# Kernel tuning notes

Measured on AMD Instinct MI355X. Metric: run time of the kernel, lower is better.

Reference implementation:

```python
import jax, jax.numpy as jnp
import numpy as np
from jax import lax

E4M3 = jnp.float8_e4m3fn
DIM_NUMS = (((1,), (0,)), ((), ()))  # contract inputs last dim with kernel first dim


def quantize_dequantize(x, q_dtype, scale, compute_dtype):
    dtype_max = jnp.finfo(q_dtype).max.astype(compute_dtype)
    s = scale.astype(compute_dtype)
    scaled = x.astype(compute_dtype) / s
    clipped = jnp.clip(scaled, -dtype_max, dtype_max)
    qx = clipped.astype(q_dtype)
    # dequantize back to x.dtype
    return qx.astype(x.dtype) * scale.astype(x.dtype)


def setup_inputs() -> dict:
    key = jax.random.key(0)
    k1, k2 = jax.random.split(key)
    H = 1024  # amax_history_length
    return {
        "inputs": jax.random.normal(k1, (8192, 4096), dtype=jnp.float32),
        "kernel": jax.random.normal(k2, (4096, 4096), dtype=jnp.float32),
        "input_scale": jnp.ones((1,), jnp.float32),
        "input_amax_history": jnp.zeros((H,), jnp.float32),
        "kernel_scale": jnp.ones((1,), jnp.float32),
        "kernel_amax_history": jnp.zeros((H,), jnp.float32),
        "output_grad_scale": jnp.ones((1,), jnp.float32),
        "output_grad_amax_history": jnp.zeros((H,), jnp.float32),
    }


def reference(inputs, kernel, input_scale, input_amax_history, kernel_scale,
              kernel_amax_history, output_grad_scale, output_grad_amax_history):
    comp_dtype = kernel.dtype
    inputs = jnp.asarray(inputs, comp_dtype)
    # in_qdq on both operands (e4m3); out_qdq is identity in the forward pass.
    lhs_qdq = quantize_dequantize(inputs, E4M3, input_scale, comp_dtype)
    rhs_qdq = quantize_dequantize(kernel, E4M3, kernel_scale, comp_dtype)
    out = lax.dot_general(lhs_qdq, rhs_qdq, DIM_NUMS, precision=None)
    return out
```

## Files before the change

kernel.cpp:

```cpp
#include <hip/hip_runtime.h>
#include <stdint.h>

#define M_DIM 8192
#define N_DIM 4096
#define K_DIM 4096
#define NT (K_DIM / 128)

typedef float f32x4 __attribute__((ext_vector_type(4)));
typedef float f32x16 __attribute__((ext_vector_type(16)));
typedef int v4i __attribute__((ext_vector_type(4)));
typedef int v8i __attribute__((ext_vector_type(8)));
typedef uint32_t u32;


__device__ __forceinline__ void gload_lds16(const void* g, void* l) {
  __builtin_amdgcn_global_load_lds(
      (__attribute__((address_space(1))) void*)(g),
      (__attribute__((address_space(3))) void*)(l), 16, 0, 0);
}

__device__ __forceinline__ float clipdiv(float v, float s) {
  v = v / s;
  return fminf(fmaxf(v, -448.f), 448.f);
}

__device__ __forceinline__ u32 pack4_fp8(float a, float b, float c, float d) {
  int w = __builtin_amdgcn_cvt_pk_fp8_f32(a, b, 0, false);
  w = __builtin_amdgcn_cvt_pk_fp8_f32(c, d, w, true);
  return (u32)w;
}

__device__ __forceinline__ v8i rd8(const void* lo, const void* hi) {
  v4i l = *(const v4i*)lo;
  v4i h = *(const v4i*)hi;
  return __builtin_shufflevector(l, h, 0, 1, 2, 3, 4, 5, 6, 7);
}

__device__ __forceinline__ f32x16 mfma32(v8i a, v8i b, f32x16 c) {
  return __builtin_amdgcn_mfma_scale_f32_32x32x64_f8f6f4(
      a, b, c, 0, 0, 0, 0x7f7f7f7f, 0, 0x7f7f7f7f);
}


__global__ __launch_bounds__(256) void quant_a(const float* __restrict__ x,
                                               u32* __restrict__ q,
                                               const float* __restrict__ scale,
                                               int nv4) {
  int base = blockIdx.x * 1024 + threadIdx.x;
  float s = scale[0];
#pragma unroll
  for (int r = 0; r < 4; ++r) {
    int idx = base + r * 256;
    if (idx < nv4) {
      float4 v = ((const float4*)x)[idx];
      q[idx] = pack4_fp8(clipdiv(v.x, s), clipdiv(v.y, s),
                         clipdiv(v.z, s), clipdiv(v.w, s));
    }
  }
}


__global__ __launch_bounds__(256) void quant_b_t(const float* __restrict__ B,
                                                 uint8_t* __restrict__ qT,
                                                 const float* __restrict__ scale) {
  __shared__ u32 lt[64 * 17];
  int tid = threadIdx.x;
  int kt = blockIdx.x * 64;
  int nt = blockIdx.y * 64;
  float s = scale[0];

  int kq = tid >> 4;
  int nq = tid & 15;
  int k0 = kq * 4, n0 = nq * 4;
  const float* src = B + (long)(kt + k0) * N_DIM + nt + n0;
  float4 v0 = *(const float4*)(src);
  float4 v1 = *(const float4*)(src + N_DIM);
  float4 v2 = *(const float4*)(src + 2 * N_DIM);
  float4 v3 = *(const float4*)(src + 3 * N_DIM);

  lt[(n0 + 0) * 17 + kq] = pack4_fp8(clipdiv(v0.x, s), clipdiv(v1.x, s),
                                     clipdiv(v2.x, s), clipdiv(v3.x, s));
  lt[(n0 + 1) * 17 + kq] = pack4_fp8(clipdiv(v0.y, s), clipdiv(v1.y, s),
                                     clipdiv(v2.y, s), clipdiv(v3.y, s));
  lt[(n0 + 2) * 17 + kq] = pack4_fp8(clipdiv(v0.z, s), clipdiv(v1.z, s),
                                     clipdiv(v2.z, s), clipdiv(v3.z, s));
  lt[(n0 + 3) * 17 + kq] = pack4_fp8(clipdiv(v0.w, s), clipdiv(v1.w, s),
                                     clipdiv(v2.w, s), clipdiv(v3.w, s));
  __syncthreads();

  int n = tid >> 2, ch = tid & 3;
  uint4 o;
  o.x = lt[n * 17 + ch * 4 + 0];
  o.y = lt[n * 17 + ch * 4 + 1];
  o.z = lt[n * 17 + ch * 4 + 2];
  o.w = lt[n * 17 + ch * 4 + 3];
  *(uint4*)&qT[(long)(nt + n) * K_DIM + kt + ch * 16] = o;
}


template <int BUF>
__device__ __forceinline__ void stage_tile(const uint8_t* const (&gA)[4],
                                           const uint8_t* const (&gB)[4],
                                           uint8_t* lds, const int (&ldo)[4],
                                           long ko) {
#pragma unroll
  for (int r = 0; r < 4; ++r)
    gload_lds16(gA[r] + ko, lds + BUF * 32768 + ldo[r]);
#pragma unroll
  for (int r = 0; r < 4; ++r)
    gload_lds16(gB[r] + ko, lds + 65536 + BUF * 32768 + ldo[r]);
}

template <int BUF>
__device__ __forceinline__ void compute_tile(const uint8_t* lds,
                                             const int (&offA)[4][4],
                                             const int (&offB)[2][4],
                                             f32x16 (&acc)[4][2]) {
  const uint8_t* Ab = lds + BUF * 32768;
  const uint8_t* Bb = lds + 65536 + BUF * 32768;
#pragma unroll
  for (int ks = 0; ks < 2; ++ks) {
    v8i b[2], a[4];
#pragma unroll
    for (int nj = 0; nj < 2; ++nj)
      b[nj] = rd8(Bb + offB[nj][ks * 2], Bb + offB[nj][ks * 2 + 1]);
#pragma unroll
    for (int mi = 0; mi < 4; ++mi)
      a[mi] = rd8(Ab + offA[mi][ks * 2], Ab + offA[mi][ks * 2 + 1]);
#pragma unroll
    for (int mi = 0; mi < 4; ++mi)
#pragma unroll
      for (int nj = 0; nj < 2; ++nj)
        acc[mi][nj] = mfma32(a[mi], b[nj], acc[mi][nj]);
  }
}

__global__ __launch_bounds__(512, 2) void gemm_mx(const uint8_t* __restrict__ Aq,
                                                  const uint8_t* __restrict__ BqT,
                                                  float* __restrict__ C,
                                                  const float* __restrict__ sA,
                                                  const float* __restrict__ sB) {
  __shared__ __align__(16) uint8_t lds[131072];

  const int tid = threadIdx.x;
  const int lane = tid & 63;
  const int wid = tid >> 6;
  const int wr = wid >> 2;
  const int wc = wid & 3;
  const int l31 = lane & 31;
  const int hi2 = lane >> 5;

  int bid = blockIdx.x;
  int wg = (bid & 7) * 64 + (bid >> 3);
  const long bm = (long)(wg >> 4) * 256;
  const long bn = (long)(wg & 15) * 256;

  float s = sA[0] * sB[0];
  asm volatile("" ::"v"(s));

  const uint8_t* gA[4];
  const uint8_t* gB[4];
  int ldo[4];
#pragma unroll
  for (int r = 0; r < 4; ++r) {
    int gid = tid + 512 * r;
    int row = gid >> 3, gc = gid & 7;
    int sc = (gc ^ (row & 7)) << 4;
    gA[r] = Aq + (bm + row) * (long)K_DIM + sc;
    gB[r] = BqT + (bn + row) * (long)K_DIM + sc;
    ldo[r] = gid * 16;
  }

  int offA[4][4], offB[2][4];
#pragma unroll
  for (int mi = 0; mi < 4; ++mi) {
    int ra = wr * 128 + mi * 32 + l31;
#pragma unroll
    for (int ks = 0; ks < 2; ++ks)
#pragma unroll
      for (int j = 0; j < 2; ++j) {
        int g = ks * 4 + hi2 * 2 + j;
        offA[mi][ks * 2 + j] = ra * 128 + ((g ^ (ra & 7)) << 4);
      }
  }
#pragma unroll
  for (int nj = 0; nj < 2; ++nj) {
    int rb = wc * 64 + nj * 32 + l31;
#pragma unroll
    for (int ks = 0; ks < 2; ++ks)
#pragma unroll
      for (int j = 0; j < 2; ++j) {
        int g = ks * 4 + hi2 * 2 + j;
        offB[nj][ks * 2 + j] = rb * 128 + ((g ^ (rb & 7)) << 4);
      }
  }

  f32x16 acc[4][2] = {};

  stage_tile<0>(gA, gB, lds, ldo, 0);
  asm volatile("s_waitcnt vmcnt(0)" ::: "memory");
  __builtin_amdgcn_s_barrier();

  for (int i = 0; i < NT / 2; ++i) {
    long ko1 = (long)((2 * i + 1) & (NT - 1)) * 128;
    stage_tile<1>(gA, gB, lds, ldo, ko1);
    compute_tile<0>(lds, offA, offB, acc);
    asm volatile("s_waitcnt vmcnt(0)" ::: "memory");
    __builtin_amdgcn_s_barrier();

    long ko2 = (long)((2 * i + 2) & (NT - 1)) * 128;
    stage_tile<0>(gA, gB, lds, ldo, ko2);
    compute_tile<1>(lds, offA, offB, acc);
    asm volatile("s_waitcnt vmcnt(0)" ::: "memory");
    __builtin_amdgcn_s_barrier();
  }

#pragma unroll
  for (int mi = 0; mi < 4; ++mi)
#pragma unroll
    for (int nj = 0; nj < 2; ++nj) {
      f32x16 v = acc[mi][nj];
      long col = bn + wc * 64 + nj * 32 + l31;
#pragma unroll
      for (int q = 0; q < 16; ++q) {
        long row = bm + wr * 128 + mi * 32 + (q & 3) + 8 * (q >> 2) + 4 * hi2;
        C[row * N_DIM + col] = v[q] * s;
      }
    }
}


extern "C" void kernel_launch(void* const* d_in, const int* in_sizes, int n_in,
                              void* d_out, int out_size, void* d_ws, size_t ws_size,
                              hipStream_t stream) {
  const float* A = (const float*)d_in[0];
  const float* B = (const float*)d_in[1];
  const float* sA = (const float*)d_in[2];
  const float* sB = (const float*)d_in[4];
  float* out = (float*)d_out;

  uint8_t* Aq = (uint8_t*)d_ws;
  uint8_t* BqT = Aq + (size_t)M_DIM * K_DIM;

  int nv4_a = M_DIM * K_DIM / 4;
  quant_a<<<nv4_a / 1024, 256, 0, stream>>>(A, (u32*)Aq, sA, nv4_a);
  quant_b_t<<<dim3(K_DIM / 64, N_DIM / 64), 256, 0, stream>>>(B, BqT, sB);
  gemm_mx<<<dim3((M_DIM / 256) * (N_DIM / 256)), 512, 0, stream>>>(Aq, BqT, out, sA, sB);
}
```

Baseline: 189.1 us.

## Interleave split global-to-LDS loads with MFMA phases using barriers and setprio

Splits each K-tile into two half-phases. Each phase issues half of the next tile's global-to-LDS loads (A first, then B), reads LDS fragments, meets at a workgroup barrier, then runs the MFMAs at raised wave priority. The aim is to spread memory traffic across the tile and keep waves in lockstep so MFMA bursts and loads from co-resident waves overlap better. The cost is extra barriers per tile and stricter scheduling constraints from sched_barrier.

```diff
diff --git a/kernel.cpp b/kernel.cpp
--- a/kernel.cpp
+++ b/kernel.cpp
@@ -99,39 +99,62 @@
 
 
 template <int BUF>
-__device__ __forceinline__ void stage_tile(const uint8_t* const (&gA)[4],
-                                           const uint8_t* const (&gB)[4],
-                                           uint8_t* lds, const int (&ldo)[4],
-                                           long ko) {
-#pragma unroll
-  for (int r = 0; r < 4; ++r)
-    gload_lds16(gA[r] + ko, lds + BUF * 32768 + ldo[r]);
-#pragma unroll
-  for (int r = 0; r < 4; ++r)
-    gload_lds16(gB[r] + ko, lds + 65536 + BUF * 32768 + ldo[r]);
-}
-
-template <int BUF>
-__device__ __forceinline__ void compute_tile(const uint8_t* lds,
-                                             const int (&offA)[4][4],
-                                             const int (&offB)[2][4],
-                                             f32x16 (&acc)[4][2]) {
+__device__ __forceinline__ void ktile(uint8_t* lds, const uint8_t* const (&gA)[4],
+                                      const uint8_t* const (&gB)[4],
+                                      const int (&ldo)[4], long ko_next,
+                                      const int (&offA)[4][4],
+                                      const int (&offB)[2][4],
+                                      f32x16 (&acc)[4][2]) {
   const uint8_t* Ab = lds + BUF * 32768;
   const uint8_t* Bb = lds + 65536 + BUF * 32768;
-#pragma unroll
-  for (int ks = 0; ks < 2; ++ks) {
-    v8i b[2], a[4];
+
+  {
+#pragma unroll
+    for (int r = 0; r < 4; ++r)
+      gload_lds16(gA[r] + ko_next, lds + (BUF ^ 1) * 32768 + ldo[r]);
+    v8i a[4], b[2];
 #pragma unroll
     for (int nj = 0; nj < 2; ++nj)
-      b[nj] = rd8(Bb + offB[nj][ks * 2], Bb + offB[nj][ks * 2 + 1]);
-#pragma unroll
-    for (int mi = 0; mi < 4; ++mi)
-      a[mi] = rd8(Ab + offA[mi][ks * 2], Ab + offA[mi][ks * 2 + 1]);
+      b[nj] = rd8(Bb + offB[nj][0], Bb + offB[nj][1]);
+#pragma unroll
+    for (int mi = 0; mi < 4; ++mi)
+      a[mi] = rd8(Ab + offA[mi][0], Ab + offA[mi][1]);
+    __builtin_amdgcn_s_barrier();
+    asm volatile("s_waitcnt lgkmcnt(0)" ::: "memory");
+    __builtin_amdgcn_sched_barrier(0);
+    __builtin_amdgcn_s_setprio(1);
 #pragma unroll
     for (int mi = 0; mi < 4; ++mi)
 #pragma unroll
       for (int nj = 0; nj < 2; ++nj)
         acc[mi][nj] = mfma32(a[mi], b[nj], acc[mi][nj]);
+    __builtin_amdgcn_s_setprio(0);
+    __builtin_amdgcn_s_barrier();
+  }
+
+  {
+#pragma unroll
+    for (int r = 0; r < 4; ++r)
+      gload_lds16(gB[r] + ko_next, lds + 65536 + (BUF ^ 1) * 32768 + ldo[r]);
+    v8i a[4], b[2];
+#pragma unroll
+    for (int nj = 0; nj < 2; ++nj)
+      b[nj] = rd8(Bb + offB[nj][2], Bb + offB[nj][3]);
+#pragma unroll
+    for (int mi = 0; mi < 4; ++mi)
+      a[mi] = rd8(Ab + offA[mi][2], Ab + offA[mi][3]);
+    __builtin_amdgcn_s_barrier();
+    asm volatile("s_waitcnt lgkmcnt(0)" ::: "memory");
+    __builtin_amdgcn_sched_barrier(0);
+    __builtin_amdgcn_s_setprio(1);
+#pragma unroll
+    for (int mi = 0; mi < 4; ++mi)
+#pragma unroll
+      for (int nj = 0; nj < 2; ++nj)
+        acc[mi][nj] = mfma32(a[mi], b[nj], acc[mi][nj]);
+    __builtin_amdgcn_s_setprio(0);
+    asm volatile("s_waitcnt vmcnt(0)" ::: "memory");
+    __builtin_amdgcn_s_barrier();
   }
 }
 
@@ -197,22 +220,18 @@
 
   f32x16 acc[4][2] = {};
 
-  stage_tile<0>(gA, gB, lds, ldo, 0);
+#pragma unroll
+  for (int r = 0; r < 4; ++r) gload_lds16(gA[r], lds + ldo[r]);
+#pragma unroll
+  for (int r = 0; r < 4; ++r) gload_lds16(gB[r], lds + 65536 + ldo[r]);
   asm volatile("s_waitcnt vmcnt(0)" ::: "memory");
   __builtin_amdgcn_s_barrier();
 
   for (int i = 0; i < NT / 2; ++i) {
     long ko1 = (long)((2 * i + 1) & (NT - 1)) * 128;
-    stage_tile<1>(gA, gB, lds, ldo, ko1);
-    compute_tile<0>(lds, offA, offB, acc);
-    asm volatile("s_waitcnt vmcnt(0)" ::: "memory");
-    __builtin_amdgcn_s_barrier();
-
     long ko2 = (long)((2 * i + 2) & (NT - 1)) * 128;
-    stage_tile<0>(gA, gB, lds, ldo, ko2);
-    compute_tile<1>(lds, offA, offB, acc);
-    asm volatile("s_waitcnt vmcnt(0)" ::: "memory");
-    __builtin_amdgcn_s_barrier();
+    ktile<0>(lds, gA, gB, ldo, ko1, offA, offB, acc);
+    ktile<1>(lds, gA, gB, ldo, ko2, offA, offB, acc);
   }
 
 #pragma unroll
```

Result: slower. 198.1 us (+4.7%).

## Load B operand directly from global into registers, halve LDS, use reciprocal scale

Applied to the files above, without the earlier changes.

The GEMM no longer stages the B tile through LDS. Each wave loads its B fragments straight from global memory into registers with double buffering, which halves the LDS footprint to 64KB and drops the B LDS reads. The quantize kernels now multiply by a precomputed reciprocal instead of dividing. The tradeoff is that B is reloaded redundantly across the two wave rows, with more global traffic and higher VGPR pressure. Multiplying by the reciprocal can also round differently from true division for scales other than one.

```diff
diff --git a/kernel.cpp b/kernel.cpp
--- a/kernel.cpp
+++ b/kernel.cpp
@@ -19,8 +19,8 @@
       (__attribute__((address_space(3))) void*)(l), 16, 0, 0);
 }
 
-__device__ __forceinline__ float clipdiv(float v, float s) {
-  v = v / s;
+__device__ __forceinline__ float clipmul(float v, float rs) {
+  v = v * rs;
   return fminf(fmaxf(v, -448.f), 448.f);
 }
 
@@ -47,14 +47,14 @@
                                                const float* __restrict__ scale,
                                                int nv4) {
   int base = blockIdx.x * 1024 + threadIdx.x;
-  float s = scale[0];
+  float rs = 1.0f / scale[0];
 #pragma unroll
   for (int r = 0; r < 4; ++r) {
     int idx = base + r * 256;
     if (idx < nv4) {
       float4 v = ((const float4*)x)[idx];
-      q[idx] = pack4_fp8(clipdiv(v.x, s), clipdiv(v.y, s),
-                         clipdiv(v.z, s), clipdiv(v.w, s));
+      q[idx] = pack4_fp8(clipmul(v.x, rs), clipmul(v.y, rs),
+                         clipmul(v.z, rs), clipmul(v.w, rs));
     }
   }
 }
@@ -67,7 +67,7 @@
   int tid = threadIdx.x;
   int kt = blockIdx.x * 64;
   int nt = blockIdx.y * 64;
-  float s = scale[0];
+  float rs = 1.0f / scale[0];
 
   int kq = tid >> 4;
   int nq = tid & 15;
@@ -78,14 +78,14 @@
   float4 v2 = *(const float4*)(src + 2 * N_DIM);
   float4 v3 = *(const float4*)(src + 3 * N_DIM);
 
-  lt[(n0 + 0) * 17 + kq] = pack4_fp8(clipdiv(v0.x, s), clipdiv(v1.x, s),
-                                     clipdiv(v2.x, s), clipdiv(v3.x, s));
-  lt[(n0 + 1) * 17 + kq] = pack4_fp8(clipdiv(v0.y, s), clipdiv(v1.y, s),
-                                     clipdiv(v2.y, s), clipdiv(v3.y, s));
-  lt[(n0 + 2) * 17 + kq] = pack4_fp8(clipdiv(v0.z, s), clipdiv(v1.z, s),
-                                     clipdiv(v2.z, s), clipdiv(v3.z, s));
-  lt[(n0 + 3) * 17 + kq] = pack4_fp8(clipdiv(v0.w, s), clipdiv(v1.w, s),
-                                     clipdiv(v2.w, s), clipdiv(v3.w, s));
+  lt[(n0 + 0) * 17 + kq] = pack4_fp8(clipmul(v0.x, rs), clipmul(v1.x, rs),
+                                     clipmul(v2.x, rs), clipmul(v3.x, rs));
+  lt[(n0 + 1) * 17 + kq] = pack4_fp8(clipmul(v0.y, rs), clipmul(v1.y, rs),
+                                     clipmul(v2.y, rs), clipmul(v3.y, rs));
+  lt[(n0 + 2) * 17 + kq] = pack4_fp8(clipmul(v0.z, rs), clipmul(v1.z, rs),
+                                     clipmul(v2.z, rs), clipmul(v3.z, rs));
+  lt[(n0 + 3) * 17 + kq] = pack4_fp8(clipmul(v0.w, rs), clipmul(v1.w, rs),
+                                     clipmul(v2.w, rs), clipmul(v3.w, rs));
   __syncthreads();
 
   int n = tid >> 2, ch = tid & 3;
@@ -99,31 +99,34 @@
 
 
 template <int BUF>
-__device__ __forceinline__ void stage_tile(const uint8_t* const (&gA)[4],
-                                           const uint8_t* const (&gB)[4],
-                                           uint8_t* lds, const int (&ldo)[4],
-                                           long ko) {
+__device__ __forceinline__ void stage_a(const uint8_t* const (&gA)[4],
+                                        uint8_t* lds, const int (&ldo)[4],
+                                        long ko) {
 #pragma unroll
   for (int r = 0; r < 4; ++r)
     gload_lds16(gA[r] + ko, lds + BUF * 32768 + ldo[r]);
-#pragma unroll
-  for (int r = 0; r < 4; ++r)
-    gload_lds16(gB[r] + ko, lds + 65536 + BUF * 32768 + ldo[r]);
+}
+
+__device__ __forceinline__ void load_b(v8i (&b)[4],
+                                       const uint8_t* const (&pB)[2], long ko) {
+#pragma unroll
+  for (int ks = 0; ks < 2; ++ks)
+#pragma unroll
+    for (int nj = 0; nj < 2; ++nj) {
+      const uint8_t* p = pB[nj] + ko + ks * 64;
+      b[ks * 2 + nj] = rd8(p, p + 16);
+    }
 }
 
 template <int BUF>
 __device__ __forceinline__ void compute_tile(const uint8_t* lds,
                                              const int (&offA)[4][4],
-                                             const int (&offB)[2][4],
+                                             const v8i (&b)[4],
                                              f32x16 (&acc)[4][2]) {
   const uint8_t* Ab = lds + BUF * 32768;
-  const uint8_t* Bb = lds + 65536 + BUF * 32768;
 #pragma unroll
   for (int ks = 0; ks < 2; ++ks) {
-    v8i b[2], a[4];
-#pragma unroll
-    for (int nj = 0; nj < 2; ++nj)
-      b[nj] = rd8(Bb + offB[nj][ks * 2], Bb + offB[nj][ks * 2 + 1]);
+    v8i a[4];
 #pragma unroll
     for (int mi = 0; mi < 4; ++mi)
       a[mi] = rd8(Ab + offA[mi][ks * 2], Ab + offA[mi][ks * 2 + 1]);
@@ -131,7 +134,7 @@
     for (int mi = 0; mi < 4; ++mi)
 #pragma unroll
       for (int nj = 0; nj < 2; ++nj)
-        acc[mi][nj] = mfma32(a[mi], b[nj], acc[mi][nj]);
+        acc[mi][nj] = mfma32(a[mi], b[ks * 2 + nj], acc[mi][nj]);
   }
 }
 
@@ -140,7 +143,7 @@
                                                   float* __restrict__ C,
                                                   const float* __restrict__ sA,
                                                   const float* __restrict__ sB) {
-  __shared__ __align__(16) uint8_t lds[131072];
+  __shared__ __align__(16) uint8_t lds[65536];
 
   const int tid = threadIdx.x;
   const int lane = tid & 63;
@@ -159,7 +162,6 @@
   asm volatile("" ::"v"(s));
 
   const uint8_t* gA[4];
-  const uint8_t* gB[4];
   int ldo[4];
 #pragma unroll
   for (int r = 0; r < 4; ++r) {
@@ -167,11 +169,10 @@
     int row = gid >> 3, gc = gid & 7;
     int sc = (gc ^ (row & 7)) << 4;
     gA[r] = Aq + (bm + row) * (long)K_DIM + sc;
-    gB[r] = BqT + (bn + row) * (long)K_DIM + sc;
     ldo[r] = gid * 16;
   }
 
-  int offA[4][4], offB[2][4];
+  int offA[4][4];
 #pragma unroll
   for (int mi = 0; mi < 4; ++mi) {
     int ra = wr * 128 + mi * 32 + l31;
@@ -183,36 +184,39 @@
         offA[mi][ks * 2 + j] = ra * 128 + ((g ^ (ra & 7)) << 4);
       }
   }
+
+  const uint8_t* pB[2];
 #pragma unroll
   for (int nj = 0; nj < 2; ++nj) {
-    int rb = wc * 64 + nj * 32 + l31;
-#pragma unroll
-    for (int ks = 0; ks < 2; ++ks)
-#pragma unroll
-      for (int j = 0; j < 2; ++j) {
-        int g = ks * 4 + hi2 * 2 + j;
-        offB[nj][ks * 2 + j] = rb * 128 + ((g ^ (rb & 7)) << 4);
-      }
+    long rb = bn + wc * 64 + nj * 32 + l31;
+    pB[nj] = BqT + rb * (long)K_DIM + hi2 * 32;
   }
 
   f32x16 acc[4][2] = {};
-
-  stage_tile<0>(gA, gB, lds, ldo, 0);
+  v8i b_even[4], b_odd[4];
+
+  stage_a<0>(gA, lds, ldo, 0);
+  load_b(b_even, pB, 0);
   asm volatile("s_waitcnt vmcnt(0)" ::: "memory");
   __builtin_amdgcn_s_barrier();
 
   for (int i = 0; i < NT / 2; ++i) {
-    long ko1 = (long)((2 * i + 1) & (NT - 1)) * 128;
-    stage_tile<1>(gA, gB, lds, ldo, ko1);
-    compute_tile<0>(lds, offA, offB, acc);
-    asm volatile("s_waitcnt vmcnt(0)" ::: "memory");
-    __builtin_amdgcn_s_barrier();
-
-    long ko2 = (long)((2 * i + 2) & (NT - 1)) * 128;
-    stage_tile<0>(gA, gB, lds, ldo, ko2);
-    compute_tile<1>(lds, offA, offB, acc);
-    asm volatile("s_waitcnt vmcnt(0)" ::: "memory");
-    __builtin_amdgcn_s_barrier();
+    {
+      long ko1 = (long)((2 * i + 1) & (NT - 1)) * 128;
+      load_b(b_odd, pB, ko1);
+      stage_a<1>(gA, lds, ldo, ko1);
+      compute_tile<0>(lds, offA, b_even, acc);
+      asm volatile("s_waitcnt vmcnt(0)" ::: "memory");
+      __builtin_amdgcn_s_barrier();
+    }
+    {
+      long ko2 = (long)((2 * i + 2) & (NT - 1)) * 128;
+      load_b(b_even, pB, ko2);
+      stage_a<0>(gA, lds, ldo, ko2);
+      compute_tile<1>(lds, offA, b_odd, acc);
+      asm volatile("s_waitcnt vmcnt(0)" ::: "memory");
+      __builtin_amdgcn_s_barrier();
+    }
   }
 
 #pragma unroll
```

Measured after the change: 268.4 us. 1.42x slower.
